# Kernel tuning notes

Hardware: AMD Instinct MI355X
Metric: run time of the kernel (lower is better)

## Reference

```python
import jax, jax.numpy as jnp
import numpy as np

DIM = 256
HEADS = 4
DIM_HEAD = 32
HIDDEN = HEADS * DIM_HEAD  # 128
GROUPS = min(DIM // 4, 32)  # 32
H = W = 256
EPS = 1e-5


def setup_inputs() -> dict:
    key = jax.random.key(0)
    ks = jax.random.split(key, 5)
    scale = 0.02
    return {
        "x": jax.random.normal(ks[0], (DIM, H, W), dtype=jnp.float32),
        "gn_weight": jnp.ones((DIM,), dtype=jnp.float32),
        "gn_bias": jnp.zeros((DIM,), dtype=jnp.float32),
        "qkv_weight": jax.random.normal(ks[1], (3 * HIDDEN, DIM), dtype=jnp.float32) * scale,
        "qkv_bias": jax.random.normal(ks[2], (3 * HIDDEN,), dtype=jnp.float32) * scale,
        "out_weight": jax.random.normal(ks[3], (DIM, HIDDEN), dtype=jnp.float32) * scale,
        "out_bias": jax.random.normal(ks[4], (DIM,), dtype=jnp.float32) * scale,
    }


def reference(x, gn_weight, gn_bias, qkv_weight, qkv_bias, out_weight, out_bias):
    c, h, w = x.shape  # (256, 256, 256)
    n = h * w

    # GroupNorm: stats per group over (channels_in_group * spatial)
    xg = x.reshape(GROUPS, -1)
    mean = jnp.mean(xg, axis=1, keepdims=True)
    var = jnp.var(xg, axis=1, keepdims=True)
    xn = ((xg - mean) * jax.lax.rsqrt(var + EPS)).reshape(c, h, w)
    xn = xn * gn_weight[:, None, None] + gn_bias[:, None, None]

    # 1x1 QKV conv -> (3*heads*dim_head, h, w), then split per rearrange layout
    qkv = jnp.einsum('oc,chw->ohw', qkv_weight, xn) + qkv_bias[:, None, None]
    qkv = qkv.reshape(3, HEADS, DIM_HEAD, n)
    q, k, v = qkv[0], qkv[1], qkv[2]

    # linear attention: softmax over spatial positions of k
    k = jax.nn.softmax(k, axis=-1)
    context = jnp.einsum('hdn,hen->hde', k, v)   # (heads, d, d) tiny
    out = jnp.einsum('hde,hdn->hen', context, q)  # (heads, d, n)
    out = out.reshape(HIDDEN, h, w)

    # 1x1 output conv
    return jnp.einsum('oc,chw->ohw', out_weight, out) + out_bias[:, None, None]
```

## Files before the change

kernel.cpp:

```cpp
#include <hip/hip_runtime.h>
#include <stdint.h>

typedef float f32x4 __attribute__((ext_vector_type(4)));
typedef short short8 __attribute__((ext_vector_type(8)));
typedef short short4v __attribute__((ext_vector_type(4)));

#define N_SPATIAL 65536

__device__ __forceinline__ float b2f(uint16_t u) {
  union { uint32_t u; float f; } v; v.u = ((uint32_t)u) << 16; return v.f;
}
__device__ __forceinline__ uint16_t f2b(float f) {
  union { float f; uint32_t u; } v; v.f = f;
  uint32_t r = (v.u + 0x7FFFu + ((v.u >> 16) & 1u)) >> 16;
  return (uint16_t)r;
}

__device__ __forceinline__ void async16(const void* g, void* l) {
  __builtin_amdgcn_global_load_lds(
      (__attribute__((address_space(1))) void*)g,
      (__attribute__((address_space(3))) void*)l, 16, 0, 0);
}

__global__ __launch_bounds__(256) void k1_transpose_stats(
    const float* __restrict__ x, uint16_t* __restrict__ xT, float* __restrict__ gnp) {
  __shared__ uint16_t xs[64][264];
  const int t = threadIdx.x;
  const int n0 = blockIdx.x * 64;
  const int c_l = (t >> 2) & 15;
  const int nq  = (t & 3) + 4 * (t >> 6);
  for (int p = 0; p < 16; ++p) {
    int c = 16 * p + c_l;
    float4 v = *(const float4*)(x + (size_t)c * N_SPATIAL + n0 + nq * 4);
    int nn = nq * 4;
    xs[nn + 0][c] = f2b(v.x); xs[nn + 1][c] = f2b(v.y);
    xs[nn + 2][c] = f2b(v.z); xs[nn + 3][c] = f2b(v.w);
  }
  __syncthreads();
  {
    int g = t >> 3; int c = g * 8 + (t & 7);
    float s = 0.f, ss = 0.f;
    for (int n = 0; n < 64; ++n) { float f = b2f(xs[n][c]); s += f; ss += f * f; }
    s  += __shfl_xor(s, 1, 64);  ss += __shfl_xor(ss, 1, 64);
    s  += __shfl_xor(s, 2, 64);  ss += __shfl_xor(ss, 2, 64);
    s  += __shfl_xor(s, 4, 64);  ss += __shfl_xor(ss, 4, 64);
    if ((t & 7) == 0) {
      gnp[((size_t)blockIdx.x * 32 + g) * 2 + 0] = s;
      gnp[((size_t)blockIdx.x * 32 + g) * 2 + 1] = ss;
    }
  }
  for (int p = 0; p < 8; ++p) {
    int j = t + 256 * p; int n = j >> 5; int c16 = j & 31;
    f32x4 val = *(const f32x4*)((const char*)&xs[0][0] + n * 528 + c16 * 16);
    *(f32x4*)((char*)xT + ((size_t)(n0 + n)) * 512 + c16 * 16) = val;
  }
}

__global__ __launch_bounds__(256) void k2_stats_final(
    const float* __restrict__ gnp, const float* __restrict__ gnw,
    const float* __restrict__ gnb, float* __restrict__ ab) {
  __shared__ float red[4][2];
  const int g = blockIdx.x; const int t = threadIdx.x;
  float s = 0.f, ss = 0.f;
  for (int c = t; c < 1024; c += 256) {
    s  += gnp[((size_t)c * 32 + g) * 2 + 0];
    ss += gnp[((size_t)c * 32 + g) * 2 + 1];
  }
  for (int m = 32; m >= 1; m >>= 1) { s += __shfl_xor(s, m, 64); ss += __shfl_xor(ss, m, 64); }
  if ((t & 63) == 0) { red[t >> 6][0] = s; red[t >> 6][1] = ss; }
  __syncthreads();
  if (t == 0) {
    float S  = red[0][0] + red[1][0] + red[2][0] + red[3][0];
    float SS = red[0][1] + red[1][1] + red[2][1] + red[3][1];
    const float invN = 1.0f / 524288.0f;
    float mean = S * invN;
    float var  = SS * invN - mean * mean;
    float rs   = rsqrtf(var + 1e-5f);
    for (int i = 0; i < 8; ++i) {
      int c = g * 8 + i;
      float aa = gnw[c] * rs;
      ab[c] = aa;
      ab[256 + c] = gnb[c] - mean * aa;
    }
  }
}

__global__ __launch_bounds__(64) void k2b_fold_w(
    const float* __restrict__ qw, const float* __restrict__ qb,
    const float* __restrict__ ab, uint16_t* __restrict__ wp, float* __restrict__ biasp) {
  const int o = blockIdx.x; const int l = threadIdx.x;
  float4 w  = *(const float4*)(qw + (size_t)o * 256 + l * 4);
  float4 av = *(const float4*)(ab + l * 4);
  float4 bv = *(const float4*)(ab + 256 + l * 4);
  short4v pk;
  pk[0] = (short)f2b(w.x * av.x); pk[1] = (short)f2b(w.y * av.y);
  pk[2] = (short)f2b(w.z * av.z); pk[3] = (short)f2b(w.w * av.w);
  *(short4v*)(wp + (size_t)o * 256 + l * 4) = pk;
  float part = w.x * bv.x + w.y * bv.y + w.z * bv.z + w.w * bv.w;
  for (int m = 32; m >= 1; m >>= 1) part += __shfl_xor(part, m, 64);
  if (l == 0) biasp[o] = qb[o] + part;
}

__global__ __launch_bounds__(256, 4) void k3_kv(
    const uint16_t* __restrict__ xT, const uint16_t* __restrict__ wp,
    const float* __restrict__ biasp, uint16_t* __restrict__ part) {
  __shared__ __align__(16) char smem[40960];
  const int t = threadIdx.x;
  const int l = t & 63, wid = t >> 6;
  const int lrow = l & 15, lk = l >> 4;

  const int n0 = blockIdx.x * 64;
  f32x4 acc[4][4] = {};
  for (int ks = 0; ks < 4; ++ks) {
    const int k0 = ks * 64;
    __syncthreads();
    #pragma unroll
    for (int it = 0; it < 8; ++it) {
      int s = it * 256 + t;
      int row = s >> 3, c = s & 7;
      const char* gsrc = (const char*)wp + (size_t)(128 + row) * 512 + k0 * 2 + ((c ^ (row & 7)) << 4);
      async16(gsrc, smem + (s & ~63) * 16);
    }
    #pragma unroll
    for (int it = 0; it < 2; ++it) {
      int s = it * 256 + t;
      int row = s >> 3, c = s & 7;
      const char* gsrc = (const char*)xT + (size_t)(n0 + row) * 512 + k0 * 2 + ((c ^ (row & 7)) << 4);
      async16(gsrc, smem + 32768 + (s & ~63) * 16);
    }
    __syncthreads();
    #pragma unroll
    for (int kk = 0; kk < 2; ++kk) {
      short8 a[4], b[4];
      #pragma unroll
      for (int m = 0; m < 4; ++m) {
        int row = wid * 64 + m * 16 + lrow;
        a[m] = *(const short8*)(&smem[row * 128 + (((kk * 4 + lk) ^ (row & 7)) << 4)]);
      }
      #pragma unroll
      for (int n = 0; n < 4; ++n) {
        int row = n * 16 + lrow;
        b[n] = *(const short8*)(&smem[32768 + row * 128 + (((kk * 4 + lk) ^ (row & 7)) << 4)]);
      }
      #pragma unroll
      for (int m = 0; m < 4; ++m)
        #pragma unroll
        for (int n = 0; n < 4; ++n)
          acc[m][n] = __builtin_amdgcn_mfma_f32_16x16x32_bf16(a[m], b[n], acc[m][n], 0, 0, 0);
    }
  }
  __syncthreads();

  float denp[16];
  #pragma unroll
  for (int i = 0; i < 16; ++i) denp[i] = 0.f;
  {
    const bool isk = wid < 2;
    const int base = isk ? 0 : 16384;
    #pragma unroll
    for (int m = 0; m < 4; ++m) {
      float bb[4];
      #pragma unroll
      for (int j = 0; j < 4; ++j) bb[j] = biasp[128 + wid * 64 + m * 16 + lk * 4 + j];
      #pragma unroll
      for (int n = 0; n < 4; ++n) {
        int col = n * 16 + lrow;
        int coff = col >> 3, cbyte = (col & 7) * 2;
        #pragma unroll
        for (int j = 0; j < 4; ++j) {
          int rloc = ((wid * 64) & 127) + m * 16 + lk * 4 + j;
          float val = acc[m][n][j] + bb[j];
          if (isk) { val = __expf(val); denp[m * 4 + j] += val; }
          *(uint16_t*)(&smem[base + rloc * 128 + ((coff ^ (rloc & 7)) << 4) + cbyte]) = f2b(val);
        }
      }
    }
  }
  __syncthreads();

  f32x4 cacc[2][2] = {};
  {
    const int h = wid;
    #pragma unroll
    for (int kw = 0; kw < 2; ++kw) {
      short8 ae[2], be[2];
      #pragma unroll
      for (int mf = 0; mf < 2; ++mf) {
        int row = h * 32 + mf * 16 + lrow;
        ae[mf] = *(const short8*)(&smem[row * 128 + (((kw * 4 + lk) ^ (row & 7)) << 4)]);
      }
      #pragma unroll
      for (int nf = 0; nf < 2; ++nf) {
        int row = h * 32 + nf * 16 + lrow;
        be[nf] = *(const short8*)(&smem[16384 + row * 128 + (((kw * 4 + lk) ^ (row & 7)) << 4)]);
      }
      #pragma unroll
      for (int mf = 0; mf < 2; ++mf)
        #pragma unroll
        for (int nf = 0; nf < 2; ++nf)
          cacc[mf][nf] = __builtin_amdgcn_mfma_f32_16x16x32_bf16(ae[mf], be[nf], cacc[mf][nf], 0, 0, 0);
    }
  }
  uint16_t* pp = part + (size_t)blockIdx.x * 4224;
  {
    uint16_t* ph = pp + wid * 1056;
    #pragma unroll
    for (int mf = 0; mf < 2; ++mf)
      #pragma unroll
      for (int nf = 0; nf < 2; ++nf)
        #pragma unroll
        for (int j = 0; j < 4; ++j) {
          int d = mf * 16 + lk * 4 + j, e = nf * 16 + lrow;
          __builtin_nontemporal_store(f2b(cacc[mf][nf][j]), &ph[d * 32 + e]);
        }
  }
  if (wid < 2) {
    #pragma unroll
    for (int i = 0; i < 16; ++i) {
      denp[i] += __shfl_xor(denp[i], 1, 64);
      denp[i] += __shfl_xor(denp[i], 2, 64);
      denp[i] += __shfl_xor(denp[i], 4, 64);
      denp[i] += __shfl_xor(denp[i], 8, 64);
    }
    if (lrow == 0) {
      #pragma unroll
      for (int m = 0; m < 4; ++m)
        #pragma unroll
        for (int j = 0; j < 4; ++j) {
          int r = wid * 64 + m * 16 + lk * 4 + j;
          __builtin_nontemporal_store(f2b(denp[m * 4 + j]),
                                      &pp[(r >> 5) * 1056 + 1024 + (r & 31)]);
        }
    }
  }
}

__global__ __launch_bounds__(256) void k6_reduce(
    const uint16_t* __restrict__ part, float* __restrict__ part2) {
  const int bx = blockIdx.x;
  const int idb = bx % 17, cg = bx / 17;
  const int id = idb * 256 + threadIdx.x;
  if (id >= 4224) return;
  const uint16_t* p = part + (size_t)cg * 128 * 4224 + id;
  float s0 = 0.f, s1 = 0.f, s2 = 0.f, s3 = 0.f;
  for (int c = 0; c < 128; c += 4) {
    s0 += b2f(p[(size_t)(c + 0) * 4224]);
    s1 += b2f(p[(size_t)(c + 1) * 4224]);
    s2 += b2f(p[(size_t)(c + 2) * 4224]);
    s3 += b2f(p[(size_t)(c + 3) * 4224]);
  }
  part2[cg * 4224 + id] = (s0 + s1) + (s2 + s3);
}

__global__ __launch_bounds__(256) void kM_fold(
    const float* __restrict__ ow, const float* __restrict__ part2,
    const uint16_t* __restrict__ wp, const float* __restrict__ biasp,
    const float* __restrict__ ob, uint16_t* __restrict__ M2,
    float* __restrict__ bias2) {
  __shared__ float sctx[4224];
  __shared__ float sow[128];
  __shared__ float smrow[128];
  __shared__ float rb[4];
  const int o = blockIdx.x; const int t = threadIdx.x;
  for (int i = t; i < 4224; i += 256) {
    float s = 0.f;
    #pragma unroll
    for (int g = 0; g < 8; ++g) s += part2[g * 4224 + i];
    sctx[i] = s;
  }
  if (t < 128) sow[t] = ow[(size_t)o * 128 + t];
  __syncthreads();
  if (t < 128) {
    int h = t >> 5, d = t & 31;
    const float* cs = sctx + h * 1056;
    float den = cs[1024 + d];
    float s = 0.f;
    #pragma unroll
    for (int e = 0; e < 32; ++e) {
      int er = (e + d) & 31;
      s += sow[h * 32 + er] * cs[d * 32 + er];
    }
    smrow[t] = s / den;
  }
  __syncthreads();
  float acc = 0.f;
  for (int d = 0; d < 128; ++d) acc += smrow[d] * b2f(wp[(size_t)d * 256 + t]);
  M2[(size_t)o * 256 + t] = f2b(acc);
  float p = (t < 128) ? smrow[t] * biasp[t] : 0.f;
  for (int m = 32; m >= 1; m >>= 1) p += __shfl_xor(p, m, 64);
  if ((t & 63) == 0) rb[t >> 6] = p;
  __syncthreads();
  if (t == 0) bias2[o] = ob[o] + rb[0] + rb[1] + rb[2] + rb[3];
}

__global__ __launch_bounds__(256, 4) void k7_out(
    const uint16_t* __restrict__ xT, const uint16_t* __restrict__ M2,
    const float* __restrict__ bias2, float* __restrict__ out) {
  __shared__ __align__(16) char smem[32768];
  const int t = threadIdx.x;
  const int ltile = (blockIdx.x & 7) * 128 + (blockIdx.x >> 3);
  const int mt = ltile & 1, nt = ltile >> 1;
  const int o0 = mt * 128, n0 = nt * 128;
  const int l = t & 63, wid = t >> 6, wr = wid >> 1, wc = wid & 1;
  const int lrow = l & 15, lk = l >> 4;

  f32x4 acc[4][4] = {};
  for (int ks = 0; ks < 4; ++ks) {
    const int k0 = ks * 64;
    __syncthreads();
    #pragma unroll
    for (int it = 0; it < 4; ++it) {
      int s = it * 256 + t;
      int row = s >> 3, c = s & 7;
      const char* gsrc = (const char*)M2 + (size_t)(o0 + row) * 512 + k0 * 2 + ((c ^ (row & 7)) << 4);
      async16(gsrc, smem + (s & ~63) * 16);
    }
    #pragma unroll
    for (int it = 0; it < 4; ++it) {
      int s = it * 256 + t;
      int row = s >> 3, c = s & 7;
      const char* gsrc = (const char*)xT + (size_t)(n0 + row) * 512 + k0 * 2 + ((c ^ (row & 7)) << 4);
      async16(gsrc, smem + 16384 + (s & ~63) * 16);
    }
    __syncthreads();
    #pragma unroll
    for (int kk = 0; kk < 2; ++kk) {
      short8 a[4], b[4];
      #pragma unroll
      for (int m = 0; m < 4; ++m) {
        int row = wr * 64 + m * 16 + lrow;
        a[m] = *(const short8*)(&smem[row * 128 + (((kk * 4 + lk) ^ (row & 7)) << 4)]);
      }
      #pragma unroll
      for (int n = 0; n < 4; ++n) {
        int row = wc * 64 + n * 16 + lrow;
        b[n] = *(const short8*)(&smem[16384 + row * 128 + (((kk * 4 + lk) ^ (row & 7)) << 4)]);
      }
      #pragma unroll
      for (int m = 0; m < 4; ++m)
        #pragma unroll
        for (int n = 0; n < 4; ++n)
          acc[m][n] = __builtin_amdgcn_mfma_f32_16x16x32_bf16(a[m], b[n], acc[m][n], 0, 0, 0);
    }
  }

  #pragma unroll
  for (int half = 0; half < 2; ++half) {
    __syncthreads();
    if (wr == half) {
      #pragma unroll
      for (int m = 0; m < 4; ++m) {
        int rb = m * 16 + lk * 4;
        float bb[4];
        #pragma unroll
        for (int j = 0; j < 4; ++j) bb[j] = bias2[o0 + half * 64 + rb + j];
        #pragma unroll
        for (int n = 0; n < 4; ++n) {
          int col = wc * 64 + n * 16 + lrow;
          #pragma unroll
          for (int j = 0; j < 4; ++j) {
            int row = rb + j;
            *(float*)(&smem[row * 512 + ((((col >> 2) ^ (row & 7)) << 4)) + (col & 3) * 4]) =
                acc[m][n][j] + bb[j];
          }
        }
      }
    }
    __syncthreads();
    #pragma unroll
    for (int p = 0; p < 8; ++p) {
      int flat = t + 256 * p; int row = flat >> 5, c = flat & 31;
      f32x4 v = *(const f32x4*)(&smem[row * 512 + (((c ^ (row & 7)) << 4))]);
      __builtin_nontemporal_store(
          v, (f32x4*)(out + (size_t)(o0 + half * 64 + row) * N_SPATIAL + n0 + c * 4));
    }
  }
}

extern "C" void kernel_launch(void* const* d_in, const int* in_sizes, int n_in,
                              void* d_out, int out_size, void* d_ws, size_t ws_size,
                              hipStream_t stream) {
  const float* x   = (const float*)d_in[0];
  const float* gnw = (const float*)d_in[1];
  const float* gnb = (const float*)d_in[2];
  const float* qw  = (const float*)d_in[3];
  const float* qb  = (const float*)d_in[4];
  const float* ow  = (const float*)d_in[5];
  const float* ob  = (const float*)d_in[6];
  float* out = (float*)d_out;
  char* ws = (char*)d_ws;

  uint16_t* xT    = (uint16_t*)(ws + 0);
  uint16_t* wp    = (uint16_t*)(ws + 33554432);
  float*    biasp = (float*)   (ws + 33751040);
  float*    ab    = (float*)   (ws + 33753088);
  float*    gnp   = (float*)   (ws + 33755136);
  uint16_t* part  = (uint16_t*)(ws + 34017280);
  float*    part2 = (float*)   (ws + 42668032);
  uint16_t* M2    = (uint16_t*)(ws + 42803200);
  float*    bias2 = (float*)   (ws + 42934272);

  k1_transpose_stats<<<dim3(1024), dim3(256), 0, stream>>>(x, xT, gnp);
  k2_stats_final<<<dim3(32), dim3(256), 0, stream>>>(gnp, gnw, gnb, ab);
  k2b_fold_w<<<dim3(384), dim3(64), 0, stream>>>(qw, qb, ab, wp, biasp);
  k3_kv<<<dim3(1024), dim3(256), 0, stream>>>(xT, wp, biasp, part);
  k6_reduce<<<dim3(136), dim3(256), 0, stream>>>(part, part2);
  kM_fold<<<dim3(256), dim3(256), 0, stream>>>(ow, part2, wp, biasp, ob, M2, bias2);
  k7_out<<<dim3(1024), dim3(256), 0, stream>>>(xT, M2, bias2, out);
}
```

Measured before the change: 83.18 us.

## Widen k3_kv tile to 128 spatial columns with 512-thread blocks

The K/V projection kernel now handles 128 spatial positions per block using 8 waves arranged 4x2. Each weight tile loaded into LDS is reused across twice as many columns, which halves total weight traffic and the block count. The context stage splits each head across two column halves and writes two partial records per block, so the partial buffer layout keeps the same total size. LDS grows to 64KB and occupancy drops to 2 blocks per CU.

```diff
diff --git a/kernel.cpp b/kernel.cpp
--- a/kernel.cpp
+++ b/kernel.cpp
@@ -101,29 +101,30 @@
   if (l == 0) biasp[o] = qb[o] + part;
 }
 
-__global__ __launch_bounds__(256, 4) void k3_kv(
+__global__ __launch_bounds__(512, 2) void k3_kv(
     const uint16_t* __restrict__ xT, const uint16_t* __restrict__ wp,
     const float* __restrict__ biasp, uint16_t* __restrict__ part) {
-  __shared__ __align__(16) char smem[40960];
+  __shared__ __align__(16) char smem[65536];
   const int t = threadIdx.x;
   const int l = t & 63, wid = t >> 6;
   const int lrow = l & 15, lk = l >> 4;
-
-  const int n0 = blockIdx.x * 64;
+  const int wr = wid >> 1, wc = wid & 1;
+
+  const int n0 = blockIdx.x * 128;
   f32x4 acc[4][4] = {};
   for (int ks = 0; ks < 4; ++ks) {
     const int k0 = ks * 64;
     __syncthreads();
     #pragma unroll
-    for (int it = 0; it < 8; ++it) {
-      int s = it * 256 + t;
+    for (int it = 0; it < 4; ++it) {
+      int s = it * 512 + t;
       int row = s >> 3, c = s & 7;
       const char* gsrc = (const char*)wp + (size_t)(128 + row) * 512 + k0 * 2 + ((c ^ (row & 7)) << 4);
       async16(gsrc, smem + (s & ~63) * 16);
     }
     #pragma unroll
     for (int it = 0; it < 2; ++it) {
-      int s = it * 256 + t;
+      int s = it * 512 + t;
       int row = s >> 3, c = s & 7;
       const char* gsrc = (const char*)xT + (size_t)(n0 + row) * 512 + k0 * 2 + ((c ^ (row & 7)) << 4);
       async16(gsrc, smem + 32768 + (s & ~63) * 16);
@@ -134,12 +135,12 @@
       short8 a[4], b[4];
       #pragma unroll
       for (int m = 0; m < 4; ++m) {
-        int row = wid * 64 + m * 16 + lrow;
+        int row = wr * 64 + m * 16 + lrow;
         a[m] = *(const short8*)(&smem[row * 128 + (((kk * 4 + lk) ^ (row & 7)) << 4)]);
       }
       #pragma unroll
       for (int n = 0; n < 4; ++n) {
-        int row = n * 16 + lrow;
+        int row = wc * 64 + n * 16 + lrow;
         b[n] = *(const short8*)(&smem[32768 + row * 128 + (((kk * 4 + lk) ^ (row & 7)) << 4)]);
       }
       #pragma unroll
@@ -155,23 +156,23 @@
   #pragma unroll
   for (int i = 0; i < 16; ++i) denp[i] = 0.f;
   {
-    const bool isk = wid < 2;
-    const int base = isk ? 0 : 16384;
+    const bool isk = wr < 2;
+    const int base = isk ? 0 : 32768;
     #pragma unroll
     for (int m = 0; m < 4; ++m) {
       float bb[4];
       #pragma unroll
-      for (int j = 0; j < 4; ++j) bb[j] = biasp[128 + wid * 64 + m * 16 + lk * 4 + j];
+      for (int j = 0; j < 4; ++j) bb[j] = biasp[128 + wr * 64 + m * 16 + lk * 4 + j];
       #pragma unroll
       for (int n = 0; n < 4; ++n) {
-        int col = n * 16 + lrow;
+        int col = wc * 64 + n * 16 + lrow;
         int coff = col >> 3, cbyte = (col & 7) * 2;
         #pragma unroll
         for (int j = 0; j < 4; ++j) {
-          int rloc = ((wid * 64) & 127) + m * 16 + lk * 4 + j;
+          int rloc = (wr & 1) * 64 + m * 16 + lk * 4 + j;
           float val = acc[m][n][j] + bb[j];
           if (isk) { val = __expf(val); denp[m * 4 + j] += val; }
-          *(uint16_t*)(&smem[base + rloc * 128 + ((coff ^ (rloc & 7)) << 4) + cbyte]) = f2b(val);
+          *(uint16_t*)(&smem[base + rloc * 256 + ((coff ^ (rloc & 7)) << 4) + cbyte]) = f2b(val);
         }
       }
     }
@@ -180,19 +181,21 @@
 
   f32x4 cacc[2][2] = {};
   {
-    const int h = wid;
+    const int h = wid & 3, ph = wid >> 2;
     #pragma unroll
     for (int kw = 0; kw < 2; ++kw) {
       short8 ae[2], be[2];
       #pragma unroll
       for (int mf = 0; mf < 2; ++mf) {
         int row = h * 32 + mf * 16 + lrow;
-        ae[mf] = *(const short8*)(&smem[row * 128 + (((kw * 4 + lk) ^ (row & 7)) << 4)]);
+        int coff = ph * 8 + kw * 4 + lk;
+        ae[mf] = *(const short8*)(&smem[row * 256 + ((coff ^ (row & 7)) << 4)]);
       }
       #pragma unroll
       for (int nf = 0; nf < 2; ++nf) {
         int row = h * 32 + nf * 16 + lrow;
-        be[nf] = *(const short8*)(&smem[16384 + row * 128 + (((kw * 4 + lk) ^ (row & 7)) << 4)]);
+        int coff = ph * 8 + kw * 4 + lk;
+        be[nf] = *(const short8*)(&smem[32768 + row * 256 + ((coff ^ (row & 7)) << 4)]);
       }
       #pragma unroll
       for (int mf = 0; mf < 2; ++mf)
@@ -201,9 +204,10 @@
           cacc[mf][nf] = __builtin_amdgcn_mfma_f32_16x16x32_bf16(ae[mf], be[nf], cacc[mf][nf], 0, 0, 0);
     }
   }
-  uint16_t* pp = part + (size_t)blockIdx.x * 4224;
+  uint16_t* pp = part + (size_t)blockIdx.x * 8448;
   {
-    uint16_t* ph = pp + wid * 1056;
+    const int h = wid & 3, ph = wid >> 2;
+    uint16_t* phd = pp + (size_t)ph * 4224 + h * 1056;
     #pragma unroll
     for (int mf = 0; mf < 2; ++mf)
       #pragma unroll
@@ -211,10 +215,10 @@
         #pragma unroll
         for (int j = 0; j < 4; ++j) {
           int d = mf * 16 + lk * 4 + j, e = nf * 16 + lrow;
-          __builtin_nontemporal_store(f2b(cacc[mf][nf][j]), &ph[d * 32 + e]);
+          __builtin_nontemporal_store(f2b(cacc[mf][nf][j]), &phd[d * 32 + e]);
         }
   }
-  if (wid < 2) {
+  if (wr < 2) {
     #pragma unroll
     for (int i = 0; i < 16; ++i) {
       denp[i] += __shfl_xor(denp[i], 1, 64);
@@ -227,9 +231,10 @@
       for (int m = 0; m < 4; ++m)
         #pragma unroll
         for (int j = 0; j < 4; ++j) {
-          int r = wid * 64 + m * 16 + lk * 4 + j;
-          __builtin_nontemporal_store(f2b(denp[m * 4 + j]),
-                                      &pp[(r >> 5) * 1056 + 1024 + (r & 31)]);
+          int r = wr * 64 + m * 16 + lk * 4 + j;
+          __builtin_nontemporal_store(
+              f2b(denp[m * 4 + j]),
+              &pp[(size_t)wc * 4224 + (r >> 5) * 1056 + 1024 + (r & 31)]);
         }
     }
   }
@@ -403,7 +408,7 @@
   k1_transpose_stats<<<dim3(1024), dim3(256), 0, stream>>>(x, xT, gnp);
   k2_stats_final<<<dim3(32), dim3(256), 0, stream>>>(gnp, gnw, gnb, ab);
   k2b_fold_w<<<dim3(384), dim3(64), 0, stream>>>(qw, qb, ab, wp, biasp);
-  k3_kv<<<dim3(1024), dim3(256), 0, stream>>>(xT, wp, biasp, part);
+  k3_kv<<<dim3(512), dim3(512), 0, stream>>>(xT, wp, biasp, part);
   k6_reduce<<<dim3(136), dim3(256), 0, stream>>>(part, part2);
   kM_fold<<<dim3(256), dim3(256), 0, stream>>>(ow, part2, wp, biasp, ob, M2, bias2);
   k7_out<<<dim3(1024), dim3(256), 0, stream>>>(xT, M2, bias2, out);
```

New measurement: 87.58 us. 5.3% more time.
